# Optimization experiments

Measured on AMD Instinct MI355X. Metric: run time of the kernel, lower is better.

Reference implementation:

```python
import jax, jax.numpy as jnp
import numpy as np

N1, N2, N3, N4 = 50_000, 100_000, 200_000, 400_000
D, OUT = 128, 128


def silu(x):
    return x * jax.nn.sigmoid(x)


def mlp(h, Wa, ba, Wb, bb):
    # torch.nn.Sequential(Linear, SiLU, Linear)
    return silu(h @ Wa + ba) @ Wb + bb


def setup_inputs() -> dict:
    key = jax.random.key(0)
    ks = jax.random.split(key, 12)
    s = 1.0 / np.sqrt(D).astype(np.float32)
    inp = {
        "feat": jax.random.normal(ks[0], (N1, D), jnp.float32),
        "W1a": jax.random.normal(ks[1], (D, D), jnp.float32) * s,
        "b1a": jnp.zeros((D,), jnp.float32),
        "W1b": jax.random.normal(ks[2], (D, D), jnp.float32) * s,
        "b1b": jnp.zeros((D,), jnp.float32),
        "W2a": jax.random.normal(ks[3], (D, D), jnp.float32) * s,
        "b2a": jnp.zeros((D,), jnp.float32),
        "W2b": jax.random.normal(ks[4], (D, D), jnp.float32) * s,
        "b2b": jnp.zeros((D,), jnp.float32),
        "W3a": jax.random.normal(ks[5], (D, D), jnp.float32) * s,
        "b3a": jnp.zeros((D,), jnp.float32),
        "W3b": jax.random.normal(ks[6], (D, D), jnp.float32) * s,
        "b3b": jnp.zeros((D,), jnp.float32),
        "Wo": jax.random.normal(ks[7], (3 * D, OUT), jnp.float32) * (1.0 / np.sqrt(3 * D).astype(np.float32)),
        "bo": jnp.zeros((OUT,), jnp.float32),
        # n{k-1}_in_n{k} edges: each level-k path has exactly 2 subpath children
        "src12": jax.random.randint(ks[8], (2 * N2,), 0, N1),
        "dst12": jnp.repeat(jnp.arange(N2), 2),
        "src23": jax.random.randint(ks[9], (2 * N3,), 0, N2),
        "dst23": jnp.repeat(jnp.arange(N3), 2),
        "src34": jax.random.randint(ks[10], (2 * N4,), 0, N3),
        "dst34": jnp.repeat(jnp.arange(N4), 2),
    }
    return inp


def reference(feat, W1a, b1a, W1b, b1b, W2a, b2a, W2b, b2b,
              W3a, b3a, W3b, b3b, Wo, bo,
              src12, dst12, src23, dst23, src34, dst34):
    # ---- upward ----
    h1 = mlp(feat, W1a, b1a, W1b, b1b)                       # n1 features (kept for final concat)
    h2 = jax.ops.segment_prod(h1[src12], dst12, num_segments=N2, indices_are_sorted=True)
    h2t = mlp(h2, W2a, b2a, W2b, b2b)
    h3 = jax.ops.segment_prod(h2t[src23], dst23, num_segments=N3, indices_are_sorted=True)
    h3t = mlp(h3, W3a, b3a, W3b, b3b)
    h4 = jax.ops.segment_prod(h3t[src34], dst34, num_segments=N4, indices_are_sorted=True)
    # ---- downward ----
    # n2_has_n1 (reverse of n1_in_n2): sum n2 features onto n1 -> 'h2'
    h2_on_n1 = jax.ops.segment_sum(h2t[dst12], src12, num_segments=N1)
    # n4_has_n3 then n3_has_n2 (overwrite h on lower level)
    h3_dn = jax.ops.segment_sum(h4[dst34], src34, num_segments=N3)
    h2_dn = jax.ops.segment_sum(h3_dn[dst23], src23, num_segments=N2)
    # n2_has_n1 again -> 'h_down'
    h_down = jax.ops.segment_sum(h2_dn[dst12], src12, num_segments=N1)
    # final per-node linear + SiLU on concat([h, h2, h_down])
    out = silu(jnp.concatenate([h1, h2_on_n1, h_down], axis=-1) @ Wo + bo)
    return out
```

## Files before the change

### kernel.cpp

```cpp
#include <hip/hip_runtime.h>

#define D 128
#define XSH 136

#define SHIFT 11
#define NPB   2048
#define EPT   8

typedef _Float16 f16;
typedef __attribute__((ext_vector_type(4))) _Float16 f16x4;
typedef __attribute__((ext_vector_type(8))) _Float16 f16x8;
typedef __attribute__((ext_vector_type(4))) float    f32x4;

__device__ __forceinline__ float silu_f(float x) {
    return x / (1.0f + __expf(-x));
}

struct WPtrs { const float* s0; const float* s1; const float* s2;
               const float* s3; const float* s4; const float* s5; };
__global__ void wconv_all_kernel(WPtrs wp, const float* __restrict__ Wo, f16* __restrict__ WT)
{
    const int blk = blockIdx.x, t = threadIdx.x;
    if (blk < 384) {
        const int wid = blk >> 6;
        const int o = ((blk & 63) << 8) + t;
        const int fi = o >> 9, r = o & 511;
        const int l = r >> 3, j = r & 7;
        const int nt = fi >> 2, kk = fi & 3;
        const int n = nt * 16 + (l & 15);
        const int k = kk * 32 + ((l >> 4) << 3) + j;
        const float* s;
        switch (wid) {
            case 0: s = wp.s0; break;
            case 1: s = wp.s1; break;
            case 2: s = wp.s2; break;
            case 3: s = wp.s3; break;
            case 4: s = wp.s4; break;
            default: s = wp.s5; break;
        }
        WT[(wid << 14) + o] = (f16)s[(k << 7) + n];
    } else {
        const int off = ((blk - 384) << 8) + t;
        const int n = off / 384, k = off - n * 384;
        WT[(6 << 14) + off] = (f16)Wo[k * 128 + n];
    }
}

template<bool GATHER>
__launch_bounds__(256)
__global__ void mlp_mfma_kernel(const void* __restrict__ in_, const int* __restrict__ src,
                                const f16* __restrict__ Wfm,
                                const float* __restrict__ ba, const float* __restrict__ bb,
                                f16* __restrict__ out, int nrows)
{
    __shared__ f16 wlds[32768];
    __shared__ f16 ys[4][2048];
    const int t = threadIdx.x;
    const int w = t >> 6, l = t & 63;
    const int cl = l & 15, kg = l >> 4;

    #pragma unroll
    for (int i = 0; i < 16; ++i) {
        const int o = (t + i * 256) * 8;
        *(f16x8*)(wlds + o) = *(const f16x8*)(Wfm + o);
    }
    __syncthreads();

    f16* ysw = ys[w];
    auto ysoff = [&](int row, int b) -> int {
        return row * 128 + ((b ^ (((row & 3) << 6) | (((row >> 2) & 3) << 4))) >> 1);
    };

    const int ntile = (nrows + 15) >> 4;
    const int stride = (int)gridDim.x * 4;
    int tile = blockIdx.x * 4 + w;
    if (tile >= ntile) return;

    f16x8 pa[4], pb[4];
    float4 pf[8];

    auto ISSUE = [&](int tl) {
        const int g = tl * 16 + cl;
        if (g >= nrows) return;
        if (GATHER) {
            const f16* in = (const f16*)in_;
            const int a = src[2 * g], b = src[2 * g + 1];
            #pragma unroll
            for (int kk = 0; kk < 4; ++kk) {
                pa[kk] = *(const f16x8*)(in + (size_t)a * D + kk * 32 + kg * 8);
                pb[kk] = *(const f16x8*)(in + (size_t)b * D + kk * 32 + kg * 8);
            }
        } else {
            const float* in = (const float*)in_;
            #pragma unroll
            for (int kk = 0; kk < 4; ++kk) {
                pf[2 * kk]     = *(const float4*)(in + (size_t)g * D + kk * 32 + kg * 8);
                pf[2 * kk + 1] = *(const float4*)(in + (size_t)g * D + kk * 32 + kg * 8 + 4);
            }
        }
    };

    ISSUE(tile);

    while (true) {
        const int nxt = tile + stride;
        const int g = tile * 16 + cl;

        f16x8 xf[4];
        if (g < nrows) {
            if (GATHER) {
                #pragma unroll
                for (int kk = 0; kk < 4; ++kk) {
                    f16x8 hv;
                    #pragma unroll
                    for (int j = 0; j < 8; ++j) hv[j] = (f16)((float)pa[kk][j] * (float)pb[kk][j]);
                    xf[kk] = hv;
                }
            } else {
                #pragma unroll
                for (int kk = 0; kk < 4; ++kk) {
                    const float4 v0 = pf[2 * kk], v1 = pf[2 * kk + 1];
                    f16x8 hv = {(f16)v0.x, (f16)v0.y, (f16)v0.z, (f16)v0.w,
                                (f16)v1.x, (f16)v1.y, (f16)v1.z, (f16)v1.w};
                    xf[kk] = hv;
                }
            }
        } else {
            f16x8 z = {};
            #pragma unroll
            for (int kk = 0; kk < 4; ++kk) xf[kk] = z;
        }

        if (nxt < ntile) ISSUE(nxt);

        f32x4 acc[8];

        #pragma unroll
        for (int nt = 0; nt < 8; ++nt) acc[nt] = (f32x4){0.f, 0.f, 0.f, 0.f};
        #pragma unroll
        for (int kk = 0; kk < 4; ++kk)
            #pragma unroll
            for (int nt = 0; nt < 8; ++nt) {
                const f16x8 wf = *(const f16x8*)(wlds + ((nt * 4 + kk) * 64 + l) * 8);
                acc[nt] = __builtin_amdgcn_mfma_f32_16x16x32_f16(wf, xf[kk], acc[nt], 0, 0, 0);
            }
        #pragma unroll
        for (int nt = 0; nt < 8; ++nt) {
            const float4 bv = *(const float4*)&ba[nt * 16 + kg * 4];
            f16x4 y;
            y[0] = (f16)silu_f(acc[nt][0] + bv.x);
            y[1] = (f16)silu_f(acc[nt][1] + bv.y);
            y[2] = (f16)silu_f(acc[nt][2] + bv.z);
            y[3] = (f16)silu_f(acc[nt][3] + bv.w);
            *(f16x4*)(ysw + ysoff(cl, nt * 32 + kg * 8)) = y;
        }
        asm volatile("s_waitcnt lgkmcnt(0)" ::: "memory");
        __builtin_amdgcn_sched_barrier(0);

        #pragma unroll
        for (int kk = 0; kk < 4; ++kk)
            xf[kk] = *(const f16x8*)(ysw + ysoff(cl, kk * 64 + kg * 16));

        #pragma unroll
        for (int nt = 0; nt < 8; ++nt) acc[nt] = (f32x4){0.f, 0.f, 0.f, 0.f};
        #pragma unroll
        for (int kk = 0; kk < 4; ++kk)
            #pragma unroll
            for (int nt = 0; nt < 8; ++nt) {
                const f16x8 wf = *(const f16x8*)(wlds + (16384 + ((nt * 4 + kk) * 64 + l) * 8));
                acc[nt] = __builtin_amdgcn_mfma_f32_16x16x32_f16(wf, xf[kk], acc[nt], 0, 0, 0);
            }
        #pragma unroll
        for (int nt = 0; nt < 8; ++nt) {
            const float4 bv = *(const float4*)&bb[nt * 16 + kg * 4];
            f16x4 z;
            z[0] = (f16)(acc[nt][0] + bv.x);
            z[1] = (f16)(acc[nt][1] + bv.y);
            z[2] = (f16)(acc[nt][2] + bv.z);
            z[3] = (f16)(acc[nt][3] + bv.w);
            *(f16x4*)(ysw + ysoff(cl, nt * 32 + kg * 8)) = z;
        }
        asm volatile("s_waitcnt lgkmcnt(0)" ::: "memory");
        __builtin_amdgcn_sched_barrier(0);

        #pragma unroll
        for (int i = 0; i < 4; ++i) {
            const int lin = i * 1024 + l * 16;
            const int row = lin >> 8, b = lin & 255;
            const int gr = tile * 16 + row;
            if (gr < nrows) {
                const f16x8 v = *(const f16x8*)(ysw + ysoff(row, b));
                *(f16x8*)(out + (size_t)gr * D + (b >> 1)) = v;
            }
        }

        if (nxt >= ntile) break;
        tile = nxt;
    }
}

__launch_bounds__(256)
__global__ void out_mfma_kernel(const f16* __restrict__ h1, const f16* __restrict__ h2t,
                                const f16* __restrict__ h2dn,
                                const int2* __restrict__ offcnt, const int* __restrict__ el,
                                const f16* __restrict__ WoT, const float* __restrict__ bo,
                                float* __restrict__ out, int nrows)
{
    __shared__ f16 xs[64][XSH];
    const int t = threadIdx.x;
    const int w = t >> 6, l = t & 63;
    const int cl = l & 15, kg = l >> 4;
    const int r = t >> 2, q = t & 3;
    const int row0 = blockIdx.x * 64;
    const int g = row0 + r;

    f32x4 acc[2][4];
    #pragma unroll
    for (int nt = 0; nt < 2; ++nt)
        #pragma unroll
        for (int m = 0; m < 4; ++m) acc[nt][m] = (f32x4){0.f, 0.f, 0.f, 0.f};

    #pragma unroll
    for (int p = 0; p < 3; ++p) {
        if (p) __syncthreads();
        {
            f16* dst = &xs[r][q * 32];
            if (g >= nrows) {
                f16x8 z = {};
                #pragma unroll
                for (int i = 0; i < 4; ++i) *(f16x8*)(dst + 8 * i) = z;
            } else if (p == 0) {
                const f16x8* pp = (const f16x8*)(h1 + (size_t)g * D + q * 32);
                #pragma unroll
                for (int i = 0; i < 4; ++i) *(f16x8*)(dst + 8 * i) = pp[i];
            } else {
                const f16* srcbuf = (p == 1) ? h2t : h2dn;
                float fa[32];
                #pragma unroll
                for (int i = 0; i < 32; ++i) fa[i] = 0.f;
                const int2 oc = offcnt[g];
                const int base = oc.x, deg = oc.y;
                int d = 0;
                for (; d + 2 <= deg; d += 2) {
                    const int j0 = el[base + d], j1 = el[base + d + 1];
                    const f16x8* p0 = (const f16x8*)(srcbuf + (size_t)j0 * D + q * 32);
                    const f16x8* p1 = (const f16x8*)(srcbuf + (size_t)j1 * D + q * 32);
                    #pragma unroll
                    for (int i = 0; i < 4; ++i) {
                        const f16x8 v0 = p0[i], v1 = p1[i];
                        #pragma unroll
                        for (int j = 0; j < 8; ++j)
                            fa[i * 8 + j] += (float)v0[j] + (float)v1[j];
                    }
                }
                if (d < deg) {
                    const int j0 = el[base + d];
                    const f16x8* p0 = (const f16x8*)(srcbuf + (size_t)j0 * D + q * 32);
                    #pragma unroll
                    for (int i = 0; i < 4; ++i) {
                        const f16x8 v0 = p0[i];
                        #pragma unroll
                        for (int j = 0; j < 8; ++j) fa[i * 8 + j] += (float)v0[j];
                    }
                }
                #pragma unroll
                for (int i = 0; i < 4; ++i) {
                    f16x8 hv;
                    #pragma unroll
                    for (int j = 0; j < 8; ++j) hv[j] = (f16)fa[i * 8 + j];
                    *(f16x8*)(dst + 8 * i) = hv;
                }
            }
        }
        __syncthreads();
        f16x8 wo[2][4];
        #pragma unroll
        for (int nt = 0; nt < 2; ++nt)
            #pragma unroll
            for (int kk = 0; kk < 4; ++kk)
                wo[nt][kk] = *(const f16x8*)(WoT + (size_t)((w * 2 + nt) * 16 + cl) * 384
                                             + p * D + kk * 32 + kg * 8);
        #pragma unroll
        for (int m = 0; m < 4; ++m)
            #pragma unroll
            for (int kk = 0; kk < 4; ++kk) {
                const f16x8 a = *(const f16x8*)&xs[m * 16 + cl][kk * 32 + kg * 8];
                acc[0][m] = __builtin_amdgcn_mfma_f32_16x16x32_f16(wo[0][kk], a, acc[0][m], 0, 0, 0);
                acc[1][m] = __builtin_amdgcn_mfma_f32_16x16x32_f16(wo[1][kk], a, acc[1][m], 0, 0, 0);
            }
    }

    #pragma unroll
    for (int nt = 0; nt < 2; ++nt) {
        const int n0 = w * 32 + nt * 16 + kg * 4;
        const float4 bv = *(const float4*)&bo[n0];
        #pragma unroll
        for (int m = 0; m < 4; ++m) {
            const int gr = row0 + m * 16 + cl;
            if (gr < nrows) {
                float4 v = make_float4(silu_f(acc[nt][m][0] + bv.x),
                                       silu_f(acc[nt][m][1] + bv.y),
                                       silu_f(acc[nt][m][2] + bv.z),
                                       silu_f(acc[nt][m][3] + bv.w));
                *(float4*)(out + (size_t)gr * D + n0) = v;
            }
        }
    }
}

__global__ void bucket_hist_kernel(const int* __restrict__ s12, int E12,
                                   const int* __restrict__ s23, int E23,
                                   const int* __restrict__ s34, int E34,
                                   int* __restrict__ bcnt, int N1, int N2, int nbkt)
{
    __shared__ int h[256];
    const int t = threadIdx.x;
    for (int i = t; i < 256; i += blockDim.x) h[i] = 0;
    __syncthreads();
    const int Etot = E12 + E23 + E34;
    for (int g = blockIdx.x * blockDim.x + t; g < Etot; g += gridDim.x * blockDim.x) {
        int node;
        if (g < E12) node = s12[g];
        else if (g < E12 + E23) node = N1 + s23[g - E12];
        else node = N1 + N2 + s34[g - E12 - E23];
        atomicAdd(&h[node >> SHIFT], 1);
    }
    __syncthreads();
    for (int i = t; i < nbkt; i += blockDim.x)
        if (h[i]) atomicAdd(&bcnt[i], h[i]);
}

__global__ void bucket_scan_kernel(const int* __restrict__ bcnt, int* __restrict__ bbase,
                                   int* __restrict__ bcur, int nbkt, int Etot)
{
    __shared__ int s[256];
    const int t = threadIdx.x;
    const int v = (t < nbkt) ? bcnt[t] : 0;
    s[t] = v;
    __syncthreads();
    for (int d = 1; d < 256; d <<= 1) {
        const int u = (t >= d) ? s[t - d] : 0;
        __syncthreads();
        s[t] += u;
        __syncthreads();
    }
    if (t < nbkt) { const int ex = s[t] - v; bbase[t] = ex; bcur[t] = ex; }
    if (t == 0) bbase[nbkt] = Etot;
}

__global__ void csr_pass1_kernel(const int* __restrict__ s12, int E12,
                                 const int* __restrict__ s23, int E23,
                                 const int* __restrict__ s34, int E34,
                                 int* __restrict__ bcur, int2* __restrict__ recs,
                                 int N1, int N2, int nbkt)
{
    __shared__ int cnt[256];
    __shared__ int gbase[256];
    const int t = threadIdx.x;
    const int chunk = blockIdx.x * (256 * EPT);
    const int Etot = E12 + E23 + E34;
    for (int i = t; i < 256; i += 256) cnt[i] = 0;
    __syncthreads();
    int node_[EPT], pay_[EPT], br_[EPT];
    #pragma unroll
    for (int i = 0; i < EPT; ++i) {
        const int g = chunk + i * 256 + t;
        int node = -1, pay = 0, b = 0, r = 0;
        if (g < Etot) {
            if (g < E12) { node = s12[g]; pay = g >> 1; }
            else if (g < E12 + E23) { const int e = g - E12; node = N1 + s23[e]; pay = e >> 1; }
            else { const int e = g - E12 - E23; node = N1 + N2 + s34[e]; pay = s34[e ^ 1]; }
            b = node >> SHIFT;
            r = atomicAdd(&cnt[b], 1);
        }
        node_[i] = node; pay_[i] = pay; br_[i] = (b << 16) | r;
    }
    __syncthreads();
    if (t < nbkt && cnt[t]) gbase[t] = atomicAdd(&bcur[t], cnt[t]);
    __syncthreads();
    #pragma unroll
    for (int i = 0; i < EPT; ++i) {
        if (node_[i] >= 0) {
            const int b = br_[i] >> 16, r = br_[i] & 0xffff;
            recs[gbase[b] + r] = make_int2(node_[i], pay_[i]);
        }
    }
}

__launch_bounds__(1024)
__global__ void csr_pass2_kernel(const int2* __restrict__ recs,
                                 const int* __restrict__ bbase,
                                 int2* __restrict__ offcnt, int* __restrict__ el, int NT)
{
    __shared__ int cnt2[NPB];
    __shared__ int pref[NPB];
    __shared__ int s1[NPB / 2];
    const int b = blockIdx.x, t = threadIdx.x;
    const int node0 = b << SHIFT;
    const int k0 = bbase[b], k1 = bbase[b + 1];
    for (int i = t; i < NPB; i += 1024) cnt2[i] = 0;
    __syncthreads();
    for (int k = k0 + t; k < k1; k += 1024)
        atomicAdd(&cnt2[recs[k].x - node0], 1);
    __syncthreads();
    s1[t] = cnt2[2 * t] + cnt2[2 * t + 1];
    __syncthreads();
    for (int d = 1; d < 1024; d <<= 1) {
        const int u = (t >= d) ? s1[t - d] : 0;
        __syncthreads();
        s1[t] += u;
        __syncthreads();
    }
    {
        const int a = cnt2[2 * t];
        const int pairsum = a + cnt2[2 * t + 1];
        const int ex0 = s1[t] - pairsum;
        pref[2 * t] = ex0;
        pref[2 * t + 1] = ex0 + a;
    }
    __syncthreads();
    for (int i = t; i < NPB; i += 1024) {
        const int node = node0 + i;
        if (node < NT) offcnt[node] = make_int2(k0 + pref[i], cnt2[i]);
    }
    __syncthreads();
    for (int k = k0 + t; k < k1; k += 1024) {
        const int2 r = recs[k];
        const int pos = atomicAdd(&pref[r.x - node0], 1);
        el[k0 + pos] = r.y;
    }
}

__global__ void prod_gather_kernel(const f16* __restrict__ h3t,
                                   const int2* __restrict__ offcnt,
                                   const int* __restrict__ el,
                                   f16* __restrict__ h3dn, int nrows)
{
    const long long g = (long long)blockIdx.x * blockDim.x + threadIdx.x;
    const int i = (int)(g >> 4);
    if (i >= nrows) return;
    const int c = ((int)g & 15) * 8;
    const f16x8 ownv = *(const f16x8*)(h3t + (size_t)i * D + c);
    float acc0[8] = {}, acc1[8] = {};
    const int2 oc = offcnt[i];
    const int base = oc.x, deg = oc.y;
    int d = 0;
    for (; d + 4 <= deg; d += 4) {
        const int s0 = el[base + d + 0], s1v = el[base + d + 1];
        const int s2 = el[base + d + 2], s3v = el[base + d + 3];
        const f16x8 v0 = *(const f16x8*)(h3t + (size_t)s0 * D + c);
        const f16x8 v1 = *(const f16x8*)(h3t + (size_t)s1v * D + c);
        const f16x8 v2 = *(const f16x8*)(h3t + (size_t)s2 * D + c);
        const f16x8 v3 = *(const f16x8*)(h3t + (size_t)s3v * D + c);
        #pragma unroll
        for (int j = 0; j < 8; ++j) {
            acc0[j] += (float)v0[j] + (float)v2[j];
            acc1[j] += (float)v1[j] + (float)v3[j];
        }
    }
    for (; d < deg; ++d) {
        const int s0 = el[base + d];
        const f16x8 v0 = *(const f16x8*)(h3t + (size_t)s0 * D + c);
        #pragma unroll
        for (int j = 0; j < 8; ++j) acc0[j] += (float)v0[j];
    }
    f16x8 r;
    #pragma unroll
    for (int j = 0; j < 8; ++j) r[j] = (f16)((acc0[j] + acc1[j]) * (float)ownv[j]);
    *(f16x8*)(h3dn + (size_t)i * D + c) = r;
}

__global__ void gather_sum_kernel(const f16* __restrict__ val,
                                  const int2* __restrict__ offcnt,
                                  const int* __restrict__ el,
                                  f16* __restrict__ dst, int nrows)
{
    const long long g = (long long)blockIdx.x * blockDim.x + threadIdx.x;
    const int i = (int)(g >> 4);
    if (i >= nrows) return;
    const int c = ((int)g & 15) * 8;
    float acc0[8] = {}, acc1[8] = {};
    const int2 oc = offcnt[i];
    const int base = oc.x, deg = oc.y;
    int d = 0;
    for (; d + 4 <= deg; d += 4) {
        const int s0 = el[base + d + 0], s1v = el[base + d + 1];
        const int s2 = el[base + d + 2], s3v = el[base + d + 3];
        const f16x8 v0 = *(const f16x8*)(val + (size_t)s0 * D + c);
        const f16x8 v1 = *(const f16x8*)(val + (size_t)s1v * D + c);
        const f16x8 v2 = *(const f16x8*)(val + (size_t)s2 * D + c);
        const f16x8 v3 = *(const f16x8*)(val + (size_t)s3v * D + c);
        #pragma unroll
        for (int j = 0; j < 8; ++j) {
            acc0[j] += (float)v0[j] + (float)v2[j];
            acc1[j] += (float)v1[j] + (float)v3[j];
        }
    }
    for (; d < deg; ++d) {
        const int s0 = el[base + d];
        const f16x8 v0 = *(const f16x8*)(val + (size_t)s0 * D + c);
        #pragma unroll
        for (int j = 0; j < 8; ++j) acc0[j] += (float)v0[j];
    }
    f16x8 r;
    #pragma unroll
    for (int j = 0; j < 8; ++j) r[j] = (f16)(acc0[j] + acc1[j]);
    *(f16x8*)(dst + (size_t)i * D + c) = r;
}

__global__ void ws_report_kernel(float* out, float v) {
    if (threadIdx.x == 0 && blockIdx.x == 0) out[0] = v;
}

extern "C" void kernel_launch(void* const* d_in, const int* in_sizes, int n_in,
                              void* d_out, int out_size, void* d_ws, size_t ws_size,
                              hipStream_t stream)
{
    const float* feat = (const float*)d_in[0];
    const float* W1a = (const float*)d_in[1];  const float* b1a = (const float*)d_in[2];
    const float* W1b = (const float*)d_in[3];  const float* b1b = (const float*)d_in[4];
    const float* W2a = (const float*)d_in[5];  const float* b2a = (const float*)d_in[6];
    const float* W2b = (const float*)d_in[7];  const float* b2b = (const float*)d_in[8];
    const float* W3a = (const float*)d_in[9];  const float* b3a = (const float*)d_in[10];
    const float* W3b = (const float*)d_in[11]; const float* b3b = (const float*)d_in[12];
    const float* Wo  = (const float*)d_in[13]; const float* bo  = (const float*)d_in[14];
    const int* src12 = (const int*)d_in[15];
    const int* src23 = (const int*)d_in[17];
    const int* src34 = (const int*)d_in[19];

    const int N1 = in_sizes[0] / D;
    const int N2 = in_sizes[15] / 2;
    const int N3 = in_sizes[17] / 2;
    const int N4 = in_sizes[19] / 2;
    const int E12 = 2 * N2, E23 = 2 * N3, E34 = 2 * N4;
    const int NT = N1 + N2 + N3;
    const int Etot = E12 + E23 + E34;
    const int NBKT = (NT + NPB - 1) >> SHIFT;

    char* p = (char*)d_ws;
    f16* h1    = (f16*)p;  p += (size_t)N1 * D * sizeof(f16);
    f16* h2t   = (f16*)p;  p += (size_t)N2 * D * sizeof(f16);
    f16* h3t   = (f16*)p;  f16* h2dn  = h3t;
    p += (size_t)N3 * D * sizeof(f16);
    f16* h3dn  = (f16*)p;
    p += (size_t)N3 * D * sizeof(f16);

    p = (char*)(((uintptr_t)p + 15) & ~(uintptr_t)15);
    int2* offcnt = (int2*)p;             p += (size_t)NT * sizeof(int2);
    int2* recs   = (int2*)p;             p += (size_t)Etot * sizeof(int2);
    int*  el     = (int*)p;              p += (size_t)Etot * sizeof(int);
    int*  bcnt   = (int*)p;              p += 256 * sizeof(int);
    int*  bbase  = (int*)p;              p += 257 * sizeof(int);
    int*  bcur   = (int*)p;              p += 256 * sizeof(int);

    p = (char*)(((uintptr_t)p + 31) & ~(uintptr_t)31);
    f16* WT = (f16*)p;
    f16* Wp1 = WT;
    f16* Wp2 = WT + 2 * 16384;
    f16* Wp3 = WT + 4 * 16384;
    f16* WoT = WT + 6 * 16384;
    p = (char*)(WoT + 384 * D);

    const size_t need = p - (char*)d_ws;
    if (ws_size < need || NBKT > 256) {
        ws_report_kernel<<<1, 64, 0, stream>>>((float*)d_out, (float)ws_size);
        return;
    }

    dim3 blk(256);
    auto rowblk16 = [](long long rows) { return dim3((unsigned)((rows * 16 + 255) / 256)); };
    auto mlpgrid  = [](int n) {
        const int nt4 = (((n + 15) >> 4) + 3) / 4;
        return dim3((unsigned)(nt4 < 512 ? nt4 : 512));
    };

    WPtrs wp = {W1a, W1b, W2a, W2b, W3a, W3b};
    wconv_all_kernel<<<dim3(576), blk, 0, stream>>>(wp, Wo, WT);

    hipMemsetAsync(bcnt, 0, 256 * sizeof(int), stream);
    {
        const int nblk = (Etot + 2047) / 2048;
        bucket_hist_kernel<<<dim3((unsigned)nblk), blk, 0, stream>>>(
            src12, E12, src23, E23, src34, E34, bcnt, N1, N2, NBKT);
        bucket_scan_kernel<<<1, 256, 0, stream>>>(bcnt, bbase, bcur, NBKT, Etot);
        csr_pass1_kernel<<<dim3((unsigned)((Etot + 256 * EPT - 1) / (256 * EPT))), blk, 0, stream>>>(
            src12, E12, src23, E23, src34, E34, bcur, recs, N1, N2, NBKT);
        csr_pass2_kernel<<<dim3((unsigned)NBKT), dim3(1024), 0, stream>>>(
            recs, bbase, offcnt, el, NT);
    }

    mlp_mfma_kernel<false><<<mlpgrid(N1), blk, 0, stream>>>(feat, nullptr, Wp1, b1a, b1b, h1, N1);
    mlp_mfma_kernel<true ><<<mlpgrid(N2), blk, 0, stream>>>(h1, src12, Wp2, b2a, b2b, h2t, N2);
    mlp_mfma_kernel<true ><<<mlpgrid(N3), blk, 0, stream>>>(h2t, src23, Wp3, b3a, b3b, h3t, N3);

    prod_gather_kernel<<<rowblk16(N3), blk, 0, stream>>>(h3t, offcnt + N1 + N2, el, h3dn, N3);
    gather_sum_kernel<<<rowblk16(N2), blk, 0, stream>>>(h3dn, offcnt + N1, el, h2dn, N2);

    out_mfma_kernel<<<dim3((unsigned)((N1 + 63) / 64)), blk, 0, stream>>>(
        h1, h2t, h2dn, offcnt, el, WoT, bo, (float*)d_out, N1);
}
```

Baseline: 248.4 us.

## Restructure output kernel to per-wave 16-row tiles without shared memory

The final output projection kernel now gives each wave its own 16-row tile. The wave builds its MFMA operands directly in registers from h1 and from the gathered h2t/h2dn sums, so the shared-memory staging and block-wide barriers are gone. Each wave computes all 128 output columns (8 accumulators) and reads Wo fragments straight from global memory or cache. The grid is capped at 512 blocks and walks the tiles in a grid-stride loop. This removes the __syncthreads stalls and LDS traffic, but each wave now loads the whole weight slice per tile and holds more registers. Each lane's gathers are also narrower 16-byte pieces scattered across the row.

```diff
diff --git a/kernel.cpp b/kernel.cpp
--- a/kernel.cpp
+++ b/kernel.cpp
@@ -1,7 +1,6 @@
 #include <hip/hip_runtime.h>
 
 #define D 128
-#define XSH 136
 
 #define SHIFT 11
 #define NPB   2048
@@ -206,103 +205,96 @@
                                 const f16* __restrict__ WoT, const float* __restrict__ bo,
                                 float* __restrict__ out, int nrows)
 {
-    __shared__ f16 xs[64][XSH];
     const int t = threadIdx.x;
     const int w = t >> 6, l = t & 63;
     const int cl = l & 15, kg = l >> 4;
-    const int r = t >> 2, q = t & 3;
-    const int row0 = blockIdx.x * 64;
-    const int g = row0 + r;
-
-    f32x4 acc[2][4];
-    #pragma unroll
-    for (int nt = 0; nt < 2; ++nt)
-        #pragma unroll
-        for (int m = 0; m < 4; ++m) acc[nt][m] = (f32x4){0.f, 0.f, 0.f, 0.f};
-
-    #pragma unroll
-    for (int p = 0; p < 3; ++p) {
-        if (p) __syncthreads();
-        {
-            f16* dst = &xs[r][q * 32];
-            if (g >= nrows) {
-                f16x8 z = {};
+    const int ntile = (nrows + 15) >> 4;
+    const int stride = (int)gridDim.x * 4;
+
+    for (int tile = blockIdx.x * 4 + w; tile < ntile; tile += stride) {
+        const int g = tile * 16 + cl;
+        const bool act = g < nrows;
+        const int2 oc = act ? offcnt[g] : make_int2(0, 0);
+
+        f32x4 acc[8];
+        #pragma unroll
+        for (int nt = 0; nt < 8; ++nt) acc[nt] = (f32x4){0.f, 0.f, 0.f, 0.f};
+
+        f16x8 xf[4];
+
+        if (act) {
+            #pragma unroll
+            for (int kk = 0; kk < 4; ++kk)
+                xf[kk] = *(const f16x8*)(h1 + (size_t)g * D + kk * 32 + kg * 8);
+        } else {
+            f16x8 z = {};
+            #pragma unroll
+            for (int kk = 0; kk < 4; ++kk) xf[kk] = z;
+        }
+        #pragma unroll
+        for (int kk = 0; kk < 4; ++kk)
+            #pragma unroll
+            for (int nt = 0; nt < 8; ++nt) {
+                const f16x8 wf = *(const f16x8*)(WoT + (size_t)(nt * 16 + cl) * 384
+                                                 + kk * 32 + kg * 8);
+                acc[nt] = __builtin_amdgcn_mfma_f32_16x16x32_f16(wf, xf[kk], acc[nt], 0, 0, 0);
+            }
+
+        #pragma unroll
+        for (int p = 1; p < 3; ++p) {
+            const f16* srcbuf = (p == 1) ? h2t : h2dn;
+            float fa[32];
+            #pragma unroll
+            for (int i = 0; i < 32; ++i) fa[i] = 0.f;
+            const int base = oc.x, deg = oc.y;
+            int d = 0;
+            for (; d + 2 <= deg; d += 2) {
+                const int j0 = el[base + d], j1 = el[base + d + 1];
                 #pragma unroll
-                for (int i = 0; i < 4; ++i) *(f16x8*)(dst + 8 * i) = z;
-            } else if (p == 0) {
-                const f16x8* pp = (const f16x8*)(h1 + (size_t)g * D + q * 32);
+                for (int kk = 0; kk < 4; ++kk) {
+                    const f16x8 v0 = *(const f16x8*)(srcbuf + (size_t)j0 * D + kk * 32 + kg * 8);
+                    const f16x8 v1 = *(const f16x8*)(srcbuf + (size_t)j1 * D + kk * 32 + kg * 8);
+                    #pragma unroll
+                    for (int j = 0; j < 8; ++j)
+                        fa[kk * 8 + j] += (float)v0[j] + (float)v1[j];
+                }
+            }
+            if (d < deg) {
+                const int j0 = el[base + d];
                 #pragma unroll
-                for (int i = 0; i < 4; ++i) *(f16x8*)(dst + 8 * i) = pp[i];
-            } else {
-                const f16* srcbuf = (p == 1) ? h2t : h2dn;
-                float fa[32];
+                for (int kk = 0; kk < 4; ++kk) {
+                    const f16x8 v0 = *(const f16x8*)(srcbuf + (size_t)j0 * D + kk * 32 + kg * 8);
+                    #pragma unroll
+                    for (int j = 0; j < 8; ++j) fa[kk * 8 + j] += (float)v0[j];
+                }
+            }
+            #pragma unroll
+            for (int kk = 0; kk < 4; ++kk) {
+                f16x8 hv;
                 #pragma unroll
-                for (int i = 0; i < 32; ++i) fa[i] = 0.f;
-                const int2 oc = offcnt[g];
-                const int base = oc.x, deg = oc.y;
-                int d = 0;
-                for (; d + 2 <= deg; d += 2) {
-                    const int j0 = el[base + d], j1 = el[base + d + 1];
-                    const f16x8* p0 = (const f16x8*)(srcbuf + (size_t)j0 * D + q * 32);
-                    const f16x8* p1 = (const f16x8*)(srcbuf + (size_t)j1 * D + q * 32);
-                    #pragma unroll
-                    for (int i = 0; i < 4; ++i) {
-                        const f16x8 v0 = p0[i], v1 = p1[i];
-                        #pragma unroll
-                        for (int j = 0; j < 8; ++j)
-                            fa[i * 8 + j] += (float)v0[j] + (float)v1[j];
-                    }
+                for (int j = 0; j < 8; ++j) hv[j] = (f16)fa[kk * 8 + j];
+                xf[kk] = hv;
+            }
+            #pragma unroll
+            for (int kk = 0; kk < 4; ++kk)
+                #pragma unroll
+                for (int nt = 0; nt < 8; ++nt) {
+                    const f16x8 wf = *(const f16x8*)(WoT + (size_t)(nt * 16 + cl) * 384
+                                                     + p * D + kk * 32 + kg * 8);
+                    acc[nt] = __builtin_amdgcn_mfma_f32_16x16x32_f16(wf, xf[kk], acc[nt], 0, 0, 0);
                 }
-                if (d < deg) {
-                    const int j0 = el[base + d];
-                    const f16x8* p0 = (const f16x8*)(srcbuf + (size_t)j0 * D + q * 32);
-                    #pragma unroll
-                    for (int i = 0; i < 4; ++i) {
-                        const f16x8 v0 = p0[i];
-                        #pragma unroll
-                        for (int j = 0; j < 8; ++j) fa[i * 8 + j] += (float)v0[j];
-                    }
-                }
-                #pragma unroll
-                for (int i = 0; i < 4; ++i) {
-                    f16x8 hv;
-                    #pragma unroll
-                    for (int j = 0; j < 8; ++j) hv[j] = (f16)fa[i * 8 + j];
-                    *(f16x8*)(dst + 8 * i) = hv;
-                }
-            }
-        }
-        __syncthreads();
-        f16x8 wo[2][4];
-        #pragma unroll
-        for (int nt = 0; nt < 2; ++nt)
-            #pragma unroll
-            for (int kk = 0; kk < 4; ++kk)
-                wo[nt][kk] = *(const f16x8*)(WoT + (size_t)((w * 2 + nt) * 16 + cl) * 384
-                                             + p * D + kk * 32 + kg * 8);
-        #pragma unroll
-        for (int m = 0; m < 4; ++m)
-            #pragma unroll
-            for (int kk = 0; kk < 4; ++kk) {
-                const f16x8 a = *(const f16x8*)&xs[m * 16 + cl][kk * 32 + kg * 8];
-                acc[0][m] = __builtin_amdgcn_mfma_f32_16x16x32_f16(wo[0][kk], a, acc[0][m], 0, 0, 0);
-                acc[1][m] = __builtin_amdgcn_mfma_f32_16x16x32_f16(wo[1][kk], a, acc[1][m], 0, 0, 0);
-            }
-    }
-
-    #pragma unroll
-    for (int nt = 0; nt < 2; ++nt) {
-        const int n0 = w * 32 + nt * 16 + kg * 4;
-        const float4 bv = *(const float4*)&bo[n0];
-        #pragma unroll
-        for (int m = 0; m < 4; ++m) {
-            const int gr = row0 + m * 16 + cl;
-            if (gr < nrows) {
-                float4 v = make_float4(silu_f(acc[nt][m][0] + bv.x),
-                                       silu_f(acc[nt][m][1] + bv.y),
-                                       silu_f(acc[nt][m][2] + bv.z),
-                                       silu_f(acc[nt][m][3] + bv.w));
-                *(float4*)(out + (size_t)gr * D + n0) = v;
+        }
+
+        if (act) {
+            #pragma unroll
+            for (int nt = 0; nt < 8; ++nt) {
+                const int n0 = nt * 16 + kg * 4;
+                const float4 bv = *(const float4*)&bo[n0];
+                float4 v = make_float4(silu_f(acc[nt][0] + bv.x),
+                                       silu_f(acc[nt][1] + bv.y),
+                                       silu_f(acc[nt][2] + bv.z),
+                                       silu_f(acc[nt][3] + bv.w));
+                *(float4*)(out + (size_t)g * D + n0) = v;
             }
         }
     }
@@ -596,6 +588,11 @@
     prod_gather_kernel<<<rowblk16(N3), blk, 0, stream>>>(h3t, offcnt + N1 + N2, el, h3dn, N3);
     gather_sum_kernel<<<rowblk16(N2), blk, 0, stream>>>(h3dn, offcnt + N1, el, h2dn, N2);
 
-    out_mfma_kernel<<<dim3((unsigned)((N1 + 63) / 64)), blk, 0, stream>>>(
-        h1, h2t, h2dn, offcnt, el, WoT, bo, (float*)d_out, N1);
-}
+    {
+        const int nt4 = ((N1 + 15) >> 4 + 3) / 4;
+        const int grid = (((N1 + 15) >> 4) + 3) / 4;
+        (void)nt4;
+        out_mfma_kernel<<<dim3((unsigned)(grid < 512 ? grid : 512)), blk, 0, stream>>>(
+            h1, h2t, h2dn, offcnt, el, WoT, bo, (float*)d_out, N1);
+    }
+}
```

Result: slower. 308.9 us (+24.3%).
